# Performance work log

Measured on AMD Instinct MI355X. Metric: run time of the kernel, lower is better.

## Reference

```python
import jax, jax.numpy as jnp
import numpy as np

EPS = 1e-15
N, DIM, H, DH = 16384, 1024, 16, 64

# ---- stereographic (k<0, hyperbolic) math, per geoopt ----

def _sabs(k):
    return jnp.clip(jnp.abs(k), EPS, None)

def _tan_k(x, k):  # k < 0 branch of geoopt tan_k
    sk = jnp.sqrt(_sabs(k))
    return jnp.tanh(x * sk) / sk

def _artan_k(x, k):  # k < 0 branch of geoopt artan_k
    sk = jnp.sqrt(_sabs(k))
    return jnp.arctanh(jnp.clip(x * sk, -1.0 + 1e-7, 1.0 - 1e-7)) / sk

def _norm(x):
    return jnp.clip(jnp.sqrt(jnp.sum(x * x, -1, keepdims=True)), EPS, None)

def _project(x, k):
    n = _norm(x)
    maxnorm = (1.0 - 1e-5) / jnp.sqrt(_sabs(k))
    return jnp.where(n > maxnorm, x / n * maxnorm, x)

def _expmap0(u, k):
    un = _norm(u)
    return _tan_k(un, k) * u / un

def _logmap0(y, k):
    yn = _norm(y)
    return _artan_k(yn, k) * y / yn

def _mobius_add(x, y, k):
    x2 = jnp.sum(x * x, -1, keepdims=True)
    y2 = jnp.sum(y * y, -1, keepdims=True)
    xy = jnp.sum(x * y, -1, keepdims=True)
    num = (1 - 2 * k * xy - k * y2) * x + (1 + k * x2) * y
    den = jnp.clip(1 - 2 * k * xy + k * k * x2 * y2, EPS, None)
    return num / den

def _mobius_scalar_mul(r, x, k):
    xn = _norm(x)
    return _tan_k(r * _artan_k(xn, k), k) * x / xn

def _clamp_abs(x, eps):
    s = jnp.where(x >= 0, 1.0, -1.0)
    return s * jnp.clip(jnp.abs(x), eps, None)

# ---- StereographicLinear: mobius_matvec + mobius bias add, per head ----

def _stereo_linear(x, W, b, c, heads):
    n, fin = x.shape
    fout = W.shape[0]
    kk = c[None, :, None]  # per-head curvature
    u = _logmap0(x.reshape(n, heads, fin // heads), kk).reshape(n, fin)
    mu = (u @ W.T).reshape(n, heads, fout // heads)
    res = _project(_expmap0(mu, kk), kk)
    sb = _project(_expmap0(b.reshape(1, heads, fout // heads), kk), kk)
    res = _project(_mobius_add(res, sb, kk), kk)
    return res.reshape(n, fout)

# ---- GeometricLinearizedAttention ----

def _linear_attn(Q, K, V, mask, c):
    # Q, K, V: [H, n, d]; mask: [n]; c: [H]
    k = c[:, None, None]
    pt = jnp.clip(1.0 + k * jnp.sum(V * V, -1, keepdims=True), EPS, None)
    v1 = Q / pt                      # parallel_transport0back(V, Q)
    v2 = K / pt                      # parallel_transport0back(V, K)
    gamma = jnp.clip(2.0 / pt, EPS, None)  # lambda_x(V)
    den = _clamp_abs(gamma - 1.0, 1e-10)
    m = mask[None, :, None]
    x = gamma / den * V * m
    v1 = jax.nn.elu(v1) + 1.0
    v2 = den * (jax.nn.elu(v2) + 1.0) * m
    v2_sum = jnp.sum(v2, axis=-2)                    # [H, d]
    Dn = jnp.einsum('hnd,hd->hn', v1, v2_sum)
    D_inv = 1.0 / jnp.where(Dn == 0, 1e-5, Dn)
    ctx = jnp.einsum('hnd,hne->hde', v2, x)          # [H, d, d]
    Xo = jnp.einsum('hde,hnd,hn->hne', ctx, v1, D_inv)
    Xo = _project(Xo, k)
    Xo = _mobius_scalar_mul(0.5, Xo, k)
    return _project(Xo, k)


def setup_inputs() -> dict:
    key = jax.random.key(0)
    ks = jax.random.split(key, 11)
    hd = H * DH
    X = jax.random.normal(ks[0], (N, DIM), jnp.float32) * 0.05  # small norms -> inside Poincare ball
    mask = (jax.random.uniform(ks[1], (N,)) > 0.1).astype(jnp.float32)
    def lin(kk, fo, fi):
        return jax.random.normal(kk, (fo, fi), jnp.float32) / np.sqrt(fi).astype(np.float32)
    Wq = lin(ks[2], hd, DIM); bq = jnp.zeros((hd,), jnp.float32)
    Wk = lin(ks[3], hd, DIM); bk = jnp.zeros((hd,), jnp.float32)
    Wv = lin(ks[4], hd, DIM); bv = jax.random.normal(ks[5], (hd,), jnp.float32) * 0.01
    Wff = lin(ks[6], DIM, hd); bff = jax.random.normal(ks[7], (DIM,), jnp.float32) * 0.01
    c_v = -(jax.random.uniform(ks[8], (H,), jnp.float32) * 0.9 + 0.1)
    c_attn = -(jax.random.uniform(ks[9], (H,), jnp.float32) * 0.9 + 0.1)
    c_ff = -(jax.random.uniform(ks[10], (H,), jnp.float32) * 0.9 + 0.1)
    return dict(X=X, mask=mask, Wq=Wq, bq=bq, Wk=Wk, bk=bk, Wv=Wv, bv=bv,
                c_v=c_v, c_attn=c_attn, Wff=Wff, bff=bff, c_ff=c_ff)


def reference(X, mask, Wq, bq, Wk, bk, Wv, bv, c_v, c_attn, Wff, bff, c_ff):
    n = X.shape[0]
    def split(t):  # [n, H*DH] -> [H, n, DH]
        return t.reshape(n, H, DH).transpose(1, 0, 2)
    Q = split(X @ Wq.T + bq)
    K = split(X @ Wk.T + bk)
    V = split(_stereo_linear(X, Wv, bv, c_v, H))
    A = _linear_attn(Q, K, V, mask, c_attn)          # [H, n, DH]
    A = A.transpose(1, 0, 2).reshape(n, H * DH)
    return _stereo_linear(A, Wff, bff, c_ff, H)
```

## Files before the change

### kernel.cpp

```cpp
#include <hip/hip_runtime.h>
#include <math.h>
#include <stdint.h>

#define NTOK 16384
#define DIMF 1024
#define NH 16
#define DHD 64
#define NQK 2048

typedef _Float16 half_t;
typedef __attribute__((ext_vector_type(8))) _Float16 half8;
typedef __attribute__((ext_vector_type(4))) _Float16 half4;
typedef __attribute__((ext_vector_type(4))) float floatx4;

__device__ __forceinline__ float wsum(float v) {
  v += __shfl_xor(v, 32, 64);
  v += __shfl_xor(v, 16, 64);
  v += __shfl_xor(v, 8, 64);
  v += __shfl_xor(v, 4, 64);
  v += __shfl_xor(v, 2, 64);
  v += __shfl_xor(v, 1, 64);
  return v;
}

template <int CTRL>
__device__ __forceinline__ float dpp_add(float v) {
  int t = __builtin_amdgcn_update_dpp(0, __float_as_int(v), CTRL, 0xF, 0xF, true);
  return v + __int_as_float(t);
}
__device__ __forceinline__ float wsum16(float v) {
  v = dpp_add<0xB1>(v);
  v = dpp_add<0x4E>(v);
  v = dpp_add<0x124>(v);
  v = dpp_add<0x128>(v);
  return v;
}

__device__ __forceinline__ float frcp(float x) { return __builtin_amdgcn_rcpf(x); }
__device__ __forceinline__ float fexp(float x) { return __expf(x); }
__device__ __forceinline__ float flog(float x) { return __logf(x); }
__device__ __forceinline__ float ftanh_pos(float x) {
  float e = fexp(2.f * x);
  return 1.f - 2.f * frcp(e + 1.f);
}
__device__ __forceinline__ float fatanh01(float t) {
  return 0.5f * flog((1.f + t) * frcp(1.f - t));
}

__device__ __forceinline__ void gload16(const void* g, void* lds) {
  __builtin_amdgcn_global_load_lds(
      (const __attribute__((address_space(1))) uint32_t*)(uintptr_t)g,
      (__attribute__((address_space(3))) uint32_t*)(uintptr_t)lds, 16, 0, 0);
}

struct EpiArgs {
  const float* sb;
  const float* y2;
  const float* c_st;
  const float* c_at;
  const float* mask;
  half_t* Qh;
  half_t* Kh;
  half_t* v2T;
  half_t* xT;
  float* v2sum;
  int qstride;
};

template <int MODE, typename OutT>
__global__ __launch_bounds__(512, 2) void gemm_f16(const half_t* __restrict__ A,
                                                   const half_t* __restrict__ B,
                                                   const float* __restrict__ bias,
                                                   OutT* __restrict__ C,
                                                   int M, int Nn, int K, EpiArgs ep) {
  __shared__ half_t sA[2][256 * 64];
  __shared__ half_t sB[2][256 * 64];
  const int tid = threadIdx.x;
  const int lane = tid & 63;
  const int w = tid >> 6;
  const int wm = w >> 2;
  const int wn = w & 3;

  int gx = gridDim.x;
  int nwg = gx * gridDim.y;
  int lin = blockIdx.y * gx + blockIdx.x;
  int bx = blockIdx.x, by = blockIdx.y;
  if ((nwg & 7) == 0) {
    int cpx = nwg >> 3;
    int swz = (lin & 7) * cpx + (lin >> 3);
    bx = swz % gx;
    by = swz / gx;
  }
  const int n0 = bx * 256;
  const int m0 = by * 256;

  const half_t* srcA[4];
  const half_t* srcB[4];
  int dstOff[4];
#pragma unroll
  for (int t = 0; t < 4; ++t) {
    int idx = w * 4 + t;
    int ks = idx >> 4, g = idx & 15;
    int row = g * 16 + (lane & 15);
    int kof = ks * 32 + (lane >> 4) * 8;
    srcA[t] = A + (size_t)(m0 + row) * K + kof;
    srcB[t] = B + (size_t)(n0 + row) * K + kof;
    dstOff[t] = (ks * 16 + g) * 512;
  }

  floatx4 acc[8][4];
#pragma unroll
  for (int i = 0; i < 8; ++i)
#pragma unroll
    for (int j = 0; j < 4; ++j) acc[i][j] = (floatx4){0.f, 0.f, 0.f, 0.f};

#pragma unroll
  for (int t = 0; t < 4; ++t) {
    gload16(srcA[t], &sA[0][dstOff[t]]);
    gload16(srcB[t], &sB[0][dstOff[t]]);
    srcA[t] += 64;
    srcB[t] += 64;
  }
  __syncthreads();

  int cur = 0;
  for (int k0 = 0; k0 < K; k0 += 64) {
    if (k0 + 64 < K) {
#pragma unroll
      for (int t = 0; t < 4; ++t) {
        gload16(srcA[t], &sA[cur ^ 1][dstOff[t]]);
        gload16(srcB[t], &sB[cur ^ 1][dstOff[t]]);
        srcA[t] += 64;
        srcB[t] += 64;
      }
    }
#pragma unroll
    for (int ks = 0; ks < 2; ++ks) {
      half8 af[8], bf[4];
#pragma unroll
      for (int i = 0; i < 8; ++i)
        af[i] = *(const half8*)&sA[cur][(ks * 16 + wm * 8 + i) * 512 + lane * 8];
#pragma unroll
      for (int j = 0; j < 4; ++j)
        bf[j] = *(const half8*)&sB[cur][(ks * 16 + wn * 4 + j) * 512 + lane * 8];
#pragma unroll
      for (int i = 0; i < 8; ++i)
#pragma unroll
        for (int j = 0; j < 4; ++j)
          acc[i][j] = __builtin_amdgcn_mfma_f32_16x16x32_f16(af[i], bf[j], acc[i][j], 0, 0, 0);
    }
    __syncthreads();
    cur ^= 1;
  }

  const int e = lane & 15;
  const int quad = lane >> 4;

  if constexpr (MODE == 0) {
#pragma unroll
    for (int j = 0; j < 4; ++j) {
      int col = n0 + wn * 64 + j * 16 + e;
      float bv = bias ? bias[col] : 0.f;
#pragma unroll
      for (int i = 0; i < 8; ++i) {
        int row = m0 + wm * 128 + i * 16 + quad * 4;
#pragma unroll
        for (int r = 0; r < 4; ++r)
          C[(size_t)(row + r) * Nn + col] = (OutT)(acc[i][j][r] + bv);
      }
    }
  } else {
    const int hb = n0 + wn * 64;
    const int h = hb >> 6;
    const float kst = ep.c_st[h];
    const float sk = sqrtf(fmaxf(fabsf(kst), 1e-15f));
    const float rsk = frcp(sk);
    const float maxn = (1.f - 1e-5f) * rsk;
    const float mx2 = maxn * maxn;
    float sbj[4];
#pragma unroll
    for (int j = 0; j < 4; ++j) sbj[j] = ep.sb[hb + j * 16 + e];
    const float y2h = ep.y2[h];
    float ka = 0.f, v2acc[4] = {0.f, 0.f, 0.f, 0.f};
    if constexpr (MODE == 1) ka = ep.c_at[h];
    const int rowbase = m0 + wm * 128;

#pragma unroll
    for (int i = 0; i < 8; ++i) {
      half4 v2s[4], xs[4];
#pragma unroll
      for (int r = 0; r < 4; ++r) {
        const int row = rowbase + i * 16 + quad * 4 + r;
        float qraw[4], kraw[4];
        float mrow = 0.f;
        size_t qb = 0;
        if constexpr (MODE == 1) {
          qb = (size_t)row * ep.qstride + hb + e;
#pragma unroll
          for (int j = 0; j < 4; ++j) {
            qraw[j] = (float)ep.Qh[qb + j * 16];
            kraw[j] = (float)ep.Kh[qb + j * 16];
          }
          mrow = ep.mask[row];
        }
        float s = 0.f, dp = 0.f;
#pragma unroll
        for (int j = 0; j < 4; ++j) {
          float mv = acc[i][j][r];
          s += mv * mv;
          dp += mv * sbj[j];
        }
        s = wsum16(s);
        dp = wsum16(dp);
        float un = fmaxf(sqrtf(s), 1e-15f);
        float tn = ftanh_pos(un * sk) * rsk;
        float f = tn * frcp(un);
        float rn = fmaxf(tn, 1e-15f);
        if (rn > maxn) { f *= maxn * frcp(rn); rn = maxn; }
        float xy = dp * f;
        float x2 = rn * rn;
        float num1 = 1.f - 2.f * kst * xy - kst * y2h;
        float num2 = 1.f + kst * x2;
        float den = fmaxf(1.f - 2.f * kst * xy + kst * kst * x2 * y2h, 1e-15f);
        float rden = frcp(den);
        float c1 = num1 * f * rden;
        float c2 = num2 * rden;
        float o[4];
        float os = 0.f;
#pragma unroll
        for (int j = 0; j < 4; ++j) {
          o[j] = c1 * acc[i][j][r] + c2 * sbj[j];
          os += o[j] * o[j];
        }
        os = wsum16(os);
        float on = fmaxf(sqrtf(os), 1e-15f);
        if (on > maxn) {
          float sc = maxn * frcp(on);
#pragma unroll
          for (int j = 0; j < 4; ++j) o[j] *= sc;
        }
        if constexpr (MODE == 2) {
#pragma unroll
          for (int j = 0; j < 4; ++j)
            C[(size_t)row * Nn + hb + j * 16 + e] = (OutT)o[j];
        } else {
          float vn2 = fminf(os, mx2);
          float pt = fmaxf(1.f + ka * vn2, 1e-15f);
          float rpt = frcp(pt);
          float gamma = fmaxf(2.f * rpt, 1e-15f);
          float gm1 = gamma - 1.f;
          float aden = fmaxf(fabsf(gm1), 1e-10f);
          float den2 = (gm1 >= 0.f) ? aden : -aden;
          float xsc = gamma * frcp(den2) * mrow;
#pragma unroll
          for (int j = 0; j < 4; ++j) {
            float q = qraw[j] * rpt;
            float v1 = (q > 0.f) ? (q + 1.f) : fexp(q);
            ep.Qh[qb + j * 16] = (half_t)v1;
            float kv = kraw[j] * rpt;
            float v2 = den2 * ((kv > 0.f) ? (kv + 1.f) : fexp(kv)) * mrow;
            v2acc[j] += v2;
            v2s[j][r] = (half_t)v2;
            xs[j][r] = (half_t)(xsc * o[j]);
          }
        }
      }
      if constexpr (MODE == 1) {
        const size_t tb0 = (size_t)(rowbase + i * 16 + quad * 4);
#pragma unroll
        for (int j = 0; j < 4; ++j) {
          size_t tb = (size_t)(hb + j * 16 + e) * NTOK + tb0;
          *(half4*)&ep.v2T[tb] = v2s[j];
          *(half4*)&ep.xT[tb] = xs[j];
        }
      }
    }
    if constexpr (MODE == 1) {
#pragma unroll
      for (int j = 0; j < 4; ++j) {
        float t = v2acc[j];
        t += __shfl_xor(t, 16, 64);
        t += __shfl_xor(t, 32, 64);
        if (quad == 0) atomicAdd(&ep.v2sum[h * DHD + j * 16 + e], t);
      }
    }
  }
}

struct WPack {
  const float* w[4];
  half_t* h[4];
};
__global__ __launch_bounds__(256) void convert_w_kernel(WPack pk) {
  int wi = blockIdx.y;
  const float* w = pk.w[wi];
  half_t* ph = pk.h[wi];
  int i = (blockIdx.x * 256 + threadIdx.x) * 4;
  float4 v = *(const float4*)&w[i];
  half4 hh = {(half_t)v.x, (half_t)v.y, (half_t)v.z, (half_t)v.w};
  *(half4*)&ph[i] = hh;
}

__global__ __launch_bounds__(128) void prep_sb_kernel(const float* __restrict__ bv,
                                                      const float* __restrict__ cv,
                                                      const float* __restrict__ bf,
                                                      const float* __restrict__ cf,
                                                      const float* __restrict__ bq,
                                                      const float* __restrict__ bk,
                                                      float* __restrict__ sbV,
                                                      float* __restrict__ y2V,
                                                      float* __restrict__ sbF,
                                                      float* __restrict__ y2F,
                                                      float* __restrict__ bqk) {
  int tid = threadIdx.x;
  for (int i = tid; i < 1024; i += 128) {
    bqk[i] = bq[i];
    bqk[1024 + i] = bk[i];
  }
  int wv = tid >> 6;
  int lane = tid & 63;
  const float* b = wv ? bf : bv;
  const float* c = wv ? cf : cv;
  float* sb = wv ? sbF : sbV;
  float* y2 = wv ? y2F : y2V;
  for (int h = 0; h < NH; ++h) {
    float k = c[h];
    float sk = sqrtf(fmaxf(fabsf(k), 1e-15f));
    float rsk = frcp(sk);
    float maxn = (1.f - 1e-5f) * rsk;
    float bb = b[h * DHD + lane];
    float bs = wsum(bb * bb);
    float bn = fmaxf(sqrtf(bs), 1e-15f);
    float tb = ftanh_pos(bn * sk) * rsk;
    float sv = tb * frcp(bn) * bb;
    float sbn = fmaxf(tb, 1e-15f);
    if (sbn > maxn) { sv *= maxn * frcp(sbn); sbn = maxn; }
    sb[h * DHD + lane] = sv;
    if (lane == 0) y2[h] = sbn * sbn;
  }
}

__global__ __launch_bounds__(256) void prep_kernel(const float* __restrict__ X,
                                                   half_t* __restrict__ Xh,
                                                   half_t* __restrict__ U,
                                                   const float* __restrict__ c) {
  int lane = threadIdx.x & 63;
  int wid = blockIdx.x * 4 + (threadIdx.x >> 6);
  int nw = gridDim.x * 4;
  int sub = lane >> 4;
  for (int row = wid; row < NTOK; row += nw) {
#pragma unroll
    for (int ch = 0; ch < 4; ++ch) {
      int h = ch * 4 + sub;
      int idx = row * DIMF + ch * 256 + lane * 4;
      float4 x = *(const float4*)&X[idx];
      float s = x.x * x.x + x.y * x.y + x.z * x.z + x.w * x.w;
      s = wsum16(s);
      float k = c[h];
      float sk = sqrtf(fmaxf(fabsf(k), 1e-15f));
      float yn = fmaxf(sqrtf(s), 1e-15f);
      float t = fminf(yn * sk, 1.f - 1e-7f);
      float f = fatanh01(t) * frcp(sk) * frcp(yn);
      half4 xh4 = {(half_t)x.x, (half_t)x.y, (half_t)x.z, (half_t)x.w};
      *(half4*)&Xh[idx] = xh4;
      half4 u4 = {(half_t)(x.x * f), (half_t)(x.y * f), (half_t)(x.z * f), (half_t)(x.w * f)};
      *(half4*)&U[idx] = u4;
    }
  }
}

__global__ __launch_bounds__(256) void attn_pass2(const half_t* __restrict__ v2T,
                                                  const half_t* __restrict__ xT,
                                                  float* __restrict__ ctxT) {
  __shared__ float red[4096];
  int tid = threadIdx.x;
  int h = blockIdx.y;
  for (int i = tid; i < 4096; i += 256) red[i] = 0.f;
  __syncthreads();
  int lane = tid & 63;
  int w = tid >> 6;
  int m = lane & 15;
  int q = lane >> 4;
  const half_t* xb = xT + (size_t)h * 64 * NTOK;
  const half_t* vb = v2T + (size_t)h * 64 * NTOK;
  floatx4 acc[4][4];
#pragma unroll
  for (int i = 0; i < 4; ++i)
#pragma unroll
    for (int j = 0; j < 4; ++j) acc[i][j] = (floatx4){0.f, 0.f, 0.f, 0.f};

  int tok0 = blockIdx.x * 512 + w * 32 + q * 8;
#pragma unroll
  for (int c = 0; c < 4; ++c) {
    int tk = tok0 + c * 128;
    half8 af[4], bf[4];
#pragma unroll
    for (int i = 0; i < 4; ++i)
      af[i] = *(const half8*)&xb[(size_t)(i * 16 + m) * NTOK + tk];
#pragma unroll
    for (int j = 0; j < 4; ++j)
      bf[j] = *(const half8*)&vb[(size_t)(j * 16 + m) * NTOK + tk];
#pragma unroll
    for (int i = 0; i < 4; ++i)
#pragma unroll
      for (int j = 0; j < 4; ++j)
        acc[i][j] = __builtin_amdgcn_mfma_f32_16x16x32_f16(af[i], bf[j], acc[i][j], 0, 0, 0);
  }
#pragma unroll
  for (int i = 0; i < 4; ++i)
#pragma unroll
    for (int j = 0; j < 4; ++j)
#pragma unroll
      for (int r = 0; r < 4; ++r) {
        int e = i * 16 + q * 4 + r;
        int d = j * 16 + m;
        atomicAdd(&red[e * 64 + d], acc[i][j][r]);
      }
  __syncthreads();
  float* dst = ctxT + (size_t)h * 4096;
  for (int i = tid; i < 4096; i += 256) atomicAdd(&dst[i], red[i]);
}

__global__ __launch_bounds__(256) void attn_pass3m(const half_t* __restrict__ v1h,
                                                   const float* __restrict__ ctxT,
                                                   const float* __restrict__ v2sum,
                                                   const float* __restrict__ c_at,
                                                   const float* __restrict__ c_ff,
                                                   half_t* __restrict__ Uff,
                                                   int sv1) {
  __shared__ half_t sctx[8 * 64 * 8];
  int tid = threadIdx.x;
  int h = blockIdx.y;
  int m0 = blockIdx.x * 64;
  for (int ci = tid; ci < 512; ci += 256) {
    int t = ci >> 6, l = ci & 63;
    int j = t & 3, ks = t >> 2;
    int e2 = j * 16 + (l & 15);
    int d = ks * 32 + (l >> 4) * 8;
    const float* src = &ctxT[h * 4096 + e2 * 64 + d];
    half8 hh;
#pragma unroll
    for (int q = 0; q < 8; ++q) hh[q] = (half_t)src[q];
    *(half8*)&sctx[ci * 8] = hh;
  }
  __syncthreads();

  int lane = tid & 63;
  int w = tid >> 6;
  int quad = lane >> 4;
  int e = lane & 15;

  const half_t* ap = v1h + (size_t)(m0 + w * 16 + e) * sv1 + h * DHD + quad * 8;
  half8 a0 = *(const half8*)ap;
  half8 a1 = *(const half8*)(ap + 32);

  const float* vsp = v2sum + h * DHD + quad * 8;
  float4 va = *(const float4*)&vsp[0];
  float4 vb = *(const float4*)&vsp[4];
  float4 vc = *(const float4*)&vsp[32];
  float4 vd = *(const float4*)&vsp[36];
  float dn = (float)a0[0] * va.x + (float)a0[1] * va.y + (float)a0[2] * va.z + (float)a0[3] * va.w +
             (float)a0[4] * vb.x + (float)a0[5] * vb.y + (float)a0[6] * vb.z + (float)a0[7] * vb.w +
             (float)a1[0] * vc.x + (float)a1[1] * vc.y + (float)a1[2] * vc.z + (float)a1[3] * vc.w +
             (float)a1[4] * vd.x + (float)a1[5] * vd.y + (float)a1[6] * vd.z + (float)a1[7] * vd.w;
  dn += __shfl_xor(dn, 16, 64);
  dn += __shfl_xor(dn, 32, 64);
  float di = frcp((dn == 0.f) ? 1e-5f : dn);

  floatx4 acc[4];
#pragma unroll
  for (int j = 0; j < 4; ++j) acc[j] = (floatx4){0.f, 0.f, 0.f, 0.f};
#pragma unroll
  for (int j = 0; j < 4; ++j) {
    half8 b0 = *(const half8*)&sctx[((0 * 4 + j) * 64 + lane) * 8];
    half8 b1 = *(const half8*)&sctx[((1 * 4 + j) * 64 + lane) * 8];
    acc[j] = __builtin_amdgcn_mfma_f32_16x16x32_f16(a0, b0, acc[j], 0, 0, 0);
    acc[j] = __builtin_amdgcn_mfma_f32_16x16x32_f16(a1, b1, acc[j], 0, 0, 0);
  }

  float ka = c_at[h];
  float sk_a = sqrtf(fmaxf(fabsf(ka), 1e-15f));
  float rsk_a = frcp(sk_a);
  float maxn_a = (1.f - 1e-5f) * rsk_a;
  float kf = c_ff[h];
  float sk_f = sqrtf(fmaxf(fabsf(kf), 1e-15f));
  float rsk_f = frcp(sk_f);

#pragma unroll
  for (int r = 0; r < 4; ++r) {
    float Di = __shfl(di, quad * 4 + r, 64);
    float v0 = acc[0][r], v1 = acc[1][r], v2 = acc[2][r], v3 = acc[3][r];
    float s = v0 * v0 + v1 * v1 + v2 * v2 + v3 * v3;
    s = wsum16(s);
    int row = m0 + w * 16 + quad * 4 + r;
    float f = Di;
    float xn = fmaxf(sqrtf(s) * Di, 1e-15f);
    if (xn > maxn_a) { f *= maxn_a * frcp(xn); xn = maxn_a; }
    float t = fminf(xn * sk_a, 1.f - 1e-7f);
    float ar = fatanh01(t) * rsk_a;
    float tk = ftanh_pos(0.5f * ar * sk_a) * rsk_a;
    f *= tk * frcp(xn);
    float nn = tk;
    if (nn > maxn_a) { f *= maxn_a * frcp(nn); nn = maxn_a; }
    float fn = fmaxf(nn, 1e-15f);
    float t2 = fminf(fn * sk_f, 1.f - 1e-7f);
    float ar2 = fatanh01(t2) * rsk_f;
    f *= ar2 * frcp(fn);
    size_t base = (size_t)row * DIMF + h * DHD + e;
    Uff[base + 0] = (half_t)(v0 * f);
    Uff[base + 16] = (half_t)(v1 * f);
    Uff[base + 32] = (half_t)(v2 * f);
    Uff[base + 48] = (half_t)(v3 * f);
  }
}

extern "C" void kernel_launch(void* const* d_in, const int* in_sizes, int n_in,
                              void* d_out, int out_size, void* d_ws, size_t ws_size,
                              hipStream_t stream) {
  const float* X = (const float*)d_in[0];
  const float* mask = (const float*)d_in[1];
  const float* Wq = (const float*)d_in[2];
  const float* bq = (const float*)d_in[3];
  const float* Wk = (const float*)d_in[4];
  const float* bk = (const float*)d_in[5];
  const float* Wv = (const float*)d_in[6];
  const float* bv = (const float*)d_in[7];
  const float* c_v = (const float*)d_in[8];
  const float* c_at = (const float*)d_in[9];
  const float* Wff = (const float*)d_in[10];
  const float* bff = (const float*)d_in[11];
  const float* c_ff = (const float*)d_in[12];
  float* out = (float*)d_out;

  const size_t NE = (size_t)NTOK * DIMF;
  float* v2sum = (float*)d_ws;
  float* ctxT = v2sum + 1024;
  float* sbV = ctxT + 65536;
  float* sbF = sbV + 1024;
  float* y2V = sbF + 1024;
  float* y2F = y2V + 16;
  float* bqk = y2F + 16;
  half_t* H1 = (half_t*)(bqk + 2048);
  half_t* H2 = H1 + NE;
  half_t* HQK = H2 + NE;
  half_t* V2T = HQK + 2 * NE;
  half_t* XT = V2T + NE;
  half_t* Wh0 = XT + NE;

  WPack pk;
  pk.w[0] = Wq; pk.w[1] = Wk; pk.w[2] = Wv; pk.w[3] = Wff;
  for (int i = 0; i < 4; ++i) pk.h[i] = Wh0 + (size_t)i * DIMF * DIMF;

  EpiArgs epN{};
  EpiArgs epV{sbV, y2V, c_v, c_at, mask, HQK, HQK + 1024, V2T, XT, v2sum, NQK};
  EpiArgs epF{sbF, y2F, c_ff, nullptr, nullptr, nullptr, nullptr, nullptr, nullptr, nullptr, 0};

  convert_w_kernel<<<dim3(1024, 4), 256, 0, stream>>>(pk);
  prep_sb_kernel<<<1, 128, 0, stream>>>(bv, c_v, bff, c_ff, bq, bk, sbV, y2V, sbF, y2F, bqk);
  prep_kernel<<<512, 256, 0, stream>>>(X, H1, H2, c_v);
  hipMemsetAsync(v2sum, 0, (1024 + 65536) * sizeof(float), stream);
  gemm_f16<0, half_t><<<dim3(NQK / 256, NTOK / 256), 512, 0, stream>>>(
      H1, pk.h[0], bqk, HQK, NTOK, NQK, DIMF, epN);
  gemm_f16<1, half_t><<<dim3(DIMF / 256, NTOK / 256), 512, 0, stream>>>(
      H2, pk.h[2], nullptr, (half_t*)nullptr, NTOK, DIMF, DIMF, epV);
  attn_pass2<<<dim3(NTOK / 512, NH), 256, 0, stream>>>(V2T, XT, ctxT);
  attn_pass3m<<<dim3(NTOK / 64, NH), 256, 0, stream>>>(HQK, ctxT, v2sum, c_at, c_ff, H1, NQK);
  gemm_f16<2, float><<<dim3(DIMF / 256, NTOK / 256), 512, 0, stream>>>(
      H1, pk.h[3], nullptr, out, NTOK, DIMF, DIMF, epF);
}
```

Baseline: 516.5 us.

## Restructure GEMM mainloop into fine-grained staged loads interleaved with MFMA phases

Replaces the simple double-buffered K loop with a four-phase schedule. Each phase loads an A/B fragment slice from LDS, issues the next global-to-LDS copy for one half-tile, and runs an MFMA burst under raised wave priority, with explicit vmcnt waits and barriers between phases. The aim is to spread global loads across the compute so memory latency is hidden and LDS stalls shrink, keeping the matrix cores busy. The price is many more barriers and a hand-tuned vmcnt count that must match the number of loads in flight, which raises the risk of a race or wrong results if the accounting is off.

```diff
diff --git a/kernel.cpp b/kernel.cpp
--- a/kernel.cpp
+++ b/kernel.cpp
@@ -94,19 +94,25 @@
   const int n0 = bx * 256;
   const int m0 = by * 256;
 
-  const half_t* srcA[4];
-  const half_t* srcB[4];
-  int dstOff[4];
-#pragma unroll
-  for (int t = 0; t < 4; ++t) {
-    int idx = w * 4 + t;
-    int ks = idx >> 4, g = idx & 15;
-    int row = g * 16 + (lane & 15);
-    int kof = ks * 32 + (lane >> 4) * 8;
-    srcA[t] = A + (size_t)(m0 + row) * K + kof;
-    srcB[t] = B + (size_t)(n0 + row) * K + kof;
-    dstOff[t] = (ks * 16 + g) * 512;
-  }
+  const half_t* pA[2];
+  const half_t* pB[2];
+#pragma unroll
+  for (int t = 0; t < 2; ++t) {
+    int g = 2 * w + t;
+    pA[t] = A + (size_t)(m0 + g * 16 + (lane & 15)) * K + ((lane >> 4) << 3);
+    pB[t] = B + (size_t)(n0 + g * 16 + (lane & 15)) * K + ((lane >> 4) << 3);
+  }
+
+  auto stageA = [&](int KS, int T, half_t* buf) {
+#pragma unroll
+    for (int t = 0; t < 2; ++t)
+      gload16(pA[t] + KS * 32 + T * 64, buf + (KS * 16 + 2 * w + t) * 512);
+  };
+  auto stageB = [&](int KS, int T, half_t* buf) {
+#pragma unroll
+    for (int t = 0; t < 2; ++t)
+      gload16(pB[t] + KS * 32 + T * 64, buf + (KS * 16 + 2 * w + t) * 512);
+  };
 
   floatx4 acc[8][4];
 #pragma unroll
@@ -114,43 +120,86 @@
 #pragma unroll
     for (int j = 0; j < 4; ++j) acc[i][j] = (floatx4){0.f, 0.f, 0.f, 0.f};
 
-#pragma unroll
-  for (int t = 0; t < 4; ++t) {
-    gload16(srcA[t], &sA[0][dstOff[t]]);
-    gload16(srcB[t], &sB[0][dstOff[t]]);
-    srcA[t] += 64;
-    srcB[t] += 64;
-  }
-  __syncthreads();
-
-  int cur = 0;
-  for (int k0 = 0; k0 < K; k0 += 64) {
-    if (k0 + 64 < K) {
-#pragma unroll
-      for (int t = 0; t < 4; ++t) {
-        gload16(srcA[t], &sA[cur ^ 1][dstOff[t]]);
-        gload16(srcB[t], &sB[cur ^ 1][dstOff[t]]);
-        srcA[t] += 64;
-        srcB[t] += 64;
-      }
-    }
-#pragma unroll
-    for (int ks = 0; ks < 2; ++ks) {
-      half8 af[8], bf[4];
-#pragma unroll
-      for (int i = 0; i < 8; ++i)
-        af[i] = *(const half8*)&sA[cur][(ks * 16 + wm * 8 + i) * 512 + lane * 8];
-#pragma unroll
-      for (int j = 0; j < 4; ++j)
-        bf[j] = *(const half8*)&sB[cur][(ks * 16 + wn * 4 + j) * 512 + lane * 8];
-#pragma unroll
-      for (int i = 0; i < 8; ++i)
-#pragma unroll
-        for (int j = 0; j < 4; ++j)
-          acc[i][j] = __builtin_amdgcn_mfma_f32_16x16x32_f16(af[i], bf[j], acc[i][j], 0, 0, 0);
-    }
-    __syncthreads();
-    cur ^= 1;
+  const int NTt = K >> 6;
+
+  stageA(0, 0, &sA[0][0]);
+  stageB(0, 0, &sB[0][0]);
+  stageA(1, 0, &sA[0][0]);
+  stageB(1, 0, &sB[0][0]);
+  stageA(0, 1, &sA[1][0]);
+  stageB(0, 1, &sB[1][0]);
+  stageA(1, 1, &sA[1][0]);
+  asm volatile("s_waitcnt vmcnt(6)" ::: "memory");
+  __builtin_amdgcn_s_barrier();
+
+  for (int kt = 0; kt < NTt; ++kt) {
+    const int c = kt & 1;
+    half_t* sAc = c ? &sA[1][0] : &sA[0][0];
+    half_t* sBc = c ? &sB[1][0] : &sB[0][0];
+    half_t* sBn = c ? &sB[0][0] : &sB[1][0];
+    half8 af[8], b0, b1;
+
+#pragma unroll
+    for (int i = 0; i < 8; ++i)
+      af[i] = *(const half8*)&sAc[(wm * 8 + i) * 512 + lane * 8];
+    b0 = *(const half8*)&sBc[(wn * 4 + 0) * 512 + lane * 8];
+    b1 = *(const half8*)&sBc[(wn * 4 + 1) * 512 + lane * 8];
+    if (kt + 1 < NTt) stageB(1, kt + 1, sBn);
+    __builtin_amdgcn_s_barrier();
+    __builtin_amdgcn_s_setprio(1);
+#pragma unroll
+    for (int i = 0; i < 8; ++i) {
+      acc[i][0] = __builtin_amdgcn_mfma_f32_16x16x32_f16(af[i], b0, acc[i][0], 0, 0, 0);
+      acc[i][1] = __builtin_amdgcn_mfma_f32_16x16x32_f16(af[i], b1, acc[i][1], 0, 0, 0);
+    }
+    __builtin_amdgcn_s_setprio(0);
+    __builtin_amdgcn_s_barrier();
+
+    b0 = *(const half8*)&sBc[(wn * 4 + 2) * 512 + lane * 8];
+    b1 = *(const half8*)&sBc[(wn * 4 + 3) * 512 + lane * 8];
+    if (kt + 2 < NTt) stageA(0, kt + 2, sAc);
+    __builtin_amdgcn_s_barrier();
+    __builtin_amdgcn_s_setprio(1);
+#pragma unroll
+    for (int i = 0; i < 8; ++i) {
+      acc[i][2] = __builtin_amdgcn_mfma_f32_16x16x32_f16(af[i], b0, acc[i][2], 0, 0, 0);
+      acc[i][3] = __builtin_amdgcn_mfma_f32_16x16x32_f16(af[i], b1, acc[i][3], 0, 0, 0);
+    }
+    __builtin_amdgcn_s_setprio(0);
+    __builtin_amdgcn_s_barrier();
+
+#pragma unroll
+    for (int i = 0; i < 8; ++i)
+      af[i] = *(const half8*)&sAc[(16 + wm * 8 + i) * 512 + lane * 8];
+    b0 = *(const half8*)&sBc[(16 + wn * 4 + 0) * 512 + lane * 8];
+    b1 = *(const half8*)&sBc[(16 + wn * 4 + 1) * 512 + lane * 8];
+    if (kt + 2 < NTt) stageB(0, kt + 2, sBc);
+    __builtin_amdgcn_s_barrier();
+    __builtin_amdgcn_s_setprio(1);
+#pragma unroll
+    for (int i = 0; i < 8; ++i) {
+      acc[i][0] = __builtin_amdgcn_mfma_f32_16x16x32_f16(af[i], b0, acc[i][0], 0, 0, 0);
+      acc[i][1] = __builtin_amdgcn_mfma_f32_16x16x32_f16(af[i], b1, acc[i][1], 0, 0, 0);
+    }
+    __builtin_amdgcn_s_setprio(0);
+    __builtin_amdgcn_s_barrier();
+
+    b0 = *(const half8*)&sBc[(16 + wn * 4 + 2) * 512 + lane * 8];
+    b1 = *(const half8*)&sBc[(16 + wn * 4 + 3) * 512 + lane * 8];
+    if (kt + 2 < NTt) stageA(1, kt + 2, sAc);
+    __builtin_amdgcn_s_barrier();
+    __builtin_amdgcn_s_setprio(1);
+#pragma unroll
+    for (int i = 0; i < 8; ++i) {
+      acc[i][2] = __builtin_amdgcn_mfma_f32_16x16x32_f16(af[i], b0, acc[i][2], 0, 0, 0);
+      acc[i][3] = __builtin_amdgcn_mfma_f32_16x16x32_f16(af[i], b1, acc[i][3], 0, 0, 0);
+    }
+    __builtin_amdgcn_s_setprio(0);
+    if (kt < NTt - 2)
+      asm volatile("s_waitcnt vmcnt(6)" ::: "memory");
+    else
+      asm volatile("s_waitcnt vmcnt(0)" ::: "memory");
+    __builtin_amdgcn_s_barrier();
   }
 
   const int e = lane & 15;
```

Result: faster. 500.3 us (median of 3 runs) (-3.1%).
